# Kernel tuning notes

Hardware: AMD Instinct MI355X
Metric: run time of the kernel (lower is better)

## Reference

```python
import jax, jax.numpy as jnp
import numpy as np

CHANNELS = 25
BN_EPS = 1e-5


def _diff(x):
    # x: [B,H,W]; zero-pad by 1 on H and W, then shifted slices (same as torch diff())
    xp = jnp.pad(x, ((0, 0), (1, 1), (1, 1)))
    p_x = (xp[:, 2:, 1:-1] - xp[:, :-2, 1:-1]) / 2
    p_y = (xp[:, 1:-1, 2:] - xp[:, 1:-1, :-2]) / 2
    pp_x = xp[:, 2:, 1:-1] + xp[:, :-2, 1:-1] - 2 * x
    pp_y = xp[:, 1:-1, 2:] + xp[:, 1:-1, :-2] - 2 * x
    pp_xy = xp[:, 2:, 2:] + xp[:, :-2, :-2] - xp[:, 2:, 1:-1] - xp[:, 1:-1, 2:]
    return p_x, p_y, pp_x, pp_y, pp_xy


def _batchnorm(x, gamma, beta):
    # x: [B,C,H,W]; training-mode BN with batch statistics (biased variance)
    mean = jnp.mean(x, axis=(0, 2, 3), keepdims=True)
    var = jnp.mean((x - mean) ** 2, axis=(0, 2, 3), keepdims=True)
    xhat = (x - mean) * jax.lax.rsqrt(var + BN_EPS)
    return xhat * gamma[None, :, None, None] + beta[None, :, None, None]


def setup_inputs() -> dict:
    key = jax.random.key(0)
    ks = jax.random.split(key, 5)
    B, H, W = 32, 512, 512
    x = jax.random.normal(ks[0], (B, H, W), dtype=jnp.float32)
    # 1x1 conv weights stored as [out_ch, in_ch]
    w1 = jax.random.normal(ks[1], (CHANNELS, 6), dtype=jnp.float32) * (1.0 / np.sqrt(6.0))
    b1 = jnp.zeros((CHANNELS,), dtype=jnp.float32)
    g1 = jnp.ones((CHANNELS,), dtype=jnp.float32)
    beta1 = jnp.zeros((CHANNELS,), dtype=jnp.float32)
    w2 = jax.random.normal(ks[2], (1, CHANNELS), dtype=jnp.float32) * (1.0 / np.sqrt(CHANNELS))
    b2 = jnp.zeros((1,), dtype=jnp.float32)
    g2 = jnp.ones((1,), dtype=jnp.float32)
    beta2 = jnp.zeros((1,), dtype=jnp.float32)
    return {"x": x, "w1": w1, "b1": b1, "g1": g1, "beta1": beta1,
            "w2": w2, "b2": b2, "g2": g2, "beta2": beta2}


def reference(x, w1, b1, g1, beta1, w2, b2, g2, beta2):
    p_x, p_y, pp_x, pp_y, pp_xy = _diff(x)
    xx = jnp.stack([x, p_x, p_y, pp_x, pp_y, pp_xy], axis=1)  # [B,6,H,W]
    # 1x1 conv == per-pixel channel matmul
    h = jnp.einsum('bchw,oc->bohw', xx, w1) + b1[None, :, None, None]
    h = jax.nn.relu(_batchnorm(h, g1, beta1))  # [B,25,H,W]
    o = jnp.einsum('bchw,oc->bohw', h, w2) + b2[None, :, None, None]
    o = jax.nn.relu(_batchnorm(o, g2, beta2))[:, 0, :, :]  # [B,H,W]
    return o + x
```

## Files before the change

kernel.cpp:

```cpp
#include <hip/hip_runtime.h>
#include <hip/hip_fp16.h>

typedef float f4 __attribute__((ext_vector_type(4)));
typedef float f2 __attribute__((ext_vector_type(2)));
typedef _Float16 f16x8 __attribute__((ext_vector_type(8)));
typedef float f32x16 __attribute__((ext_vector_type(16)));

#define NPIX (32*512*512)
#define BN_EPS 1e-5f


__global__ __launch_bounds__(256) void k_moments(const float* __restrict__ x,
                                                 const float* __restrict__ ws,
                                                 float* __restrict__ outp) {
    __shared__ ushort sl[4][8][64];
    __shared__ float mom[4][7][7];
    int t = threadIdx.x;
    int l = t & 63, wv = t >> 6;
    int h = l >> 5;
    const float* zb = ws + 1024;

    sl[wv][6][l] = (ushort)0x3C00;
    sl[wv][7][l] = (ushort)0;

    f32x16 accA, accB;
    #pragma unroll
    for (int r = 0; r < 16; ++r) { accA[r] = 0.f; accB[r] = 0.f; }

    int arow = ((l & 31) < 7) ? (l & 31) : 7;
    const ushort* rdp = &sl[wv][arow][8*h];

    int wave_id = blockIdx.x * 4 + wv;
    #pragma unroll 1
    for (int rr = 0; rr < 2; ++rr) {
        int row = wave_id * 2 + rr;
        int i = row & 511;
        const float* xr = x + row * 512;
        const float* xn = (i > 0)   ? xr - 512 : zb;
        const float* xs = (i < 511) ? xr + 512 : zb;
        #pragma unroll 1
        for (int it = 0; it < 8; ++it) {
            int col = it * 64 + l;
            bool okw = (col > 0), oke = (col < 511);
            int cm = okw ? col - 1 : 0;
            int cp = oke ? col + 1 : 511;
            float C  = xr[col], N = xn[col], S_ = xs[col];
            float W_ = xr[cm],  E = xr[cp];
            float NW = xn[cm],  SE = xs[cp];
            W_ = okw ? W_ : 0.f; NW = okw ? NW : 0.f;
            E  = oke ? E  : 0.f; SE = oke ? SE : 0.f;

            float s0 = C;
            float s1 = (S_ - N) * 0.5f;
            float s2 = (E - W_) * 0.5f;
            float s3 = S_ + N - 2.f*C;
            float s4 = E + W_ - 2.f*C;
            float s5 = SE + NW - S_ - E;

            __half h0 = __float2half(s0), h1 = __float2half(s1);
            __half h2 = __float2half(s2), h3 = __float2half(s3);
            __half h4 = __float2half(s4), h5 = __float2half(s5);
            sl[wv][0][l] = *(ushort*)&h0;
            sl[wv][1][l] = *(ushort*)&h1;
            sl[wv][2][l] = *(ushort*)&h2;
            sl[wv][3][l] = *(ushort*)&h3;
            sl[wv][4][l] = *(ushort*)&h4;
            sl[wv][5][l] = *(ushort*)&h5;
            __builtin_amdgcn_wave_barrier();

            union { uint4 u; f16x8 v; } f0, f1, f2_, f3;
            f0.u  = *(const uint4*)(rdp);
            f1.u  = *(const uint4*)(rdp + 16);
            f2_.u = *(const uint4*)(rdp + 32);
            f3.u  = *(const uint4*)(rdp + 48);
            accA = __builtin_amdgcn_mfma_f32_32x32x16_f16(f0.v,  f0.v,  accA, 0, 0, 0);
            accB = __builtin_amdgcn_mfma_f32_32x32x16_f16(f1.v,  f1.v,  accB, 0, 0, 0);
            accA = __builtin_amdgcn_mfma_f32_32x32x16_f16(f2_.v, f2_.v, accA, 0, 0, 0);
            accB = __builtin_amdgcn_mfma_f32_32x32x16_f16(f3.v,  f3.v,  accB, 0, 0, 0);
            __builtin_amdgcn_wave_barrier();
        }
    }

    if ((l & 31) < 7) {
        int j = l & 31;
        #pragma unroll
        for (int r = 0; r < 4; ++r) {
            int irow = r + 4*h;
            if (irow < 7) mom[wv][irow][j] = accA[r] + accB[r];
        }
    }
    __syncthreads();
    if (t < 27) {
        int a, b;
        if (t < 6) { a = t; b = 6; }
        else {
            int rem = t - 6; a = 0;
            while (rem >= 6 - a) { rem -= 6 - a; ++a; }
            b = a + rem;
        }
        float v = mom[0][a][b] + mom[1][a][b] + mom[2][a][b] + mom[3][a][b];
        outp[t*2048 + blockIdx.x] = v;
    }
}

__global__ __launch_bounds__(256) void k_red(const float* __restrict__ outp,
                                             float* __restrict__ ws) {
    int b = blockIdx.x;
    int t = threadIdx.x;
    float v = 0.f;
    #pragma unroll
    for (int k = 0; k < 8; ++k) v += outp[b*2048 + t + 256*k];
    for (int off = 32; off; off >>= 1) v += __shfl_xor(v, off);
    __shared__ float red[4];
    int wave = t >> 6, lane = t & 63;
    if (lane == 0) red[wave] = v;
    __syncthreads();
    if (t == 0) ws[b] = red[0] + red[1] + red[2] + red[3];
}

__global__ void k_stats1(const float* w1, const float* b1, const float* g1,
                         const float* beta1, const float* w2, float* ws) {
    __shared__ float sm[32][8];
    int c = threadIdx.x;
    if (c < 32) {
        #pragma unroll
        for (int k = 0; k < 8; ++k) sm[c][k] = 0.f;
        ws[64 + c] = (c < 25) ? w2[c] : 0.f;
    }
    __syncthreads();
    if (c < 25) {
        const float invN = 1.f / (float)NPIX;
        float m1[6], wr[6];
        #pragma unroll
        for (int i = 0; i < 6; ++i) m1[i] = ws[i] * invN;
        #pragma unroll
        for (int i = 0; i < 6; ++i) wr[i] = w1[c*6 + i];
        float bc = b1[c];
        float mean = bc;
        #pragma unroll
        for (int i = 0; i < 6; ++i) mean = fmaf(wr[i], m1[i], mean);
        float e2 = bc * bc;
        #pragma unroll
        for (int i = 0; i < 6; ++i) e2 = fmaf(2.f*bc*wr[i], m1[i], e2);
        #pragma unroll
        for (int i = 0; i < 6; ++i)
            #pragma unroll
            for (int j = 0; j < 6; ++j) {
                int a = i < j ? i : j, b = i < j ? j : i;
                float m2 = ws[6 + a*(11-a)/2 + b] * invN;
                e2 = fmaf(wr[i]*wr[j], m2, e2);
            }
        float var = e2 - mean*mean;
        float a1 = g1[c] * rsqrtf(var + BN_EPS);
        #pragma unroll
        for (int i = 0; i < 6; ++i) sm[c][i] = a1 * wr[i];
        sm[c][6] = fmaf(a1, bc - mean, beta1[c]);
    }
    __syncthreads();
    int ch = c & 31, h = c >> 5;
    float aC=0.f, aN=0.f, aS=0.f, aE=0.f, aW=0.f, aNW=0.f, aSE=0.f, ab=0.f;
    if (h == 0) {
        float w0 = sm[ch][0], w1v = sm[ch][1], w2v = sm[ch][2];
        float w3 = sm[ch][3], w4v = sm[ch][4], w5 = sm[ch][5], be = sm[ch][6];
        aC  = w0 - 2.f*w3 - 2.f*w4v;
        aN  = -0.5f*w1v + w3;
        aS  =  0.5f*w1v + w3 - w5;
        aE  =  0.5f*w2v + w4v - w5;
        aW  = -0.5f*w2v + w4v;
        aNW = w5;
        aSE = w5;
        ab  = be;
    }
    __half2 p0 = __floats2half2_rn(aC,  aN);
    __half2 p1 = __floats2half2_rn(aS,  aE);
    __half2 p2 = __floats2half2_rn(aW,  aNW);
    __half2 p3 = __floats2half2_rn(aSE, ab);
    unsigned u0, u1, u2, u3;
    __builtin_memcpy(&u0, &p0, 4);
    __builtin_memcpy(&u1, &p1, 4);
    __builtin_memcpy(&u2, &p2, 4);
    __builtin_memcpy(&u3, &p3, 4);
    uint4 fr = {u0, u1, u2, u3};
    ((uint4*)(ws + 96))[c] = fr;
}

__global__ __launch_bounds__(256) void k_main(const float* __restrict__ x,
                                              const float* __restrict__ ws,
                                              const float* __restrict__ b2,
                                              float* __restrict__ stats,
                                              float* __restrict__ opre) {
    int t = threadIdx.x;
    int l = t & 63, wv = t >> 6;
    int lane31 = l & 31, h = l >> 5;
    const float* zb = ws + 1024;

    f16x8 afr;
    {
        uint4 u = ((const uint4*)(ws + 96))[l];
        union { uint4 u; f16x8 v; } cv; cv.u = u; afr = cv.v;
    }
    f2 w2p[8];
    #pragma unroll
    for (int r2 = 0; r2 < 8; ++r2) {
        int creg = ((2*r2) & 3) + 8 * ((2*r2) >> 2) + 4*h;
        w2p[r2] = *(const f2*)(ws + 64 + creg);
    }
    f32x16 zacc;
    #pragma unroll
    for (int r = 0; r < 16; ++r) zacc[r] = 0.f;
    float b2v = b2[0];
    float S1 = 0.f, S2 = 0.f;

    int wave_id = blockIdx.x * 4 + wv;
    #pragma unroll 1
    for (int rr = 0; rr < 2; ++rr) {
        int row = wave_id * 2 + rr;
        int i = row & 511;
        const float* xc = x + row * 512 + lane31;
        const float* xn = (i > 0)   ? xc - 512 : zb + lane31;
        const float* xs = (i < 511) ? xc + 512 : zb + lane31;
        float* op = opre + row * 512 + lane31;

        #pragma unroll
        for (int jt = 0; jt < 16; ++jt) {
            const int o4 = jt * 32;
            int offm1 = o4 - 1, offp1 = o4 + 1;
            if (jt == 0  && lane31 == 0)  offm1 = o4;
            if (jt == 15 && lane31 == 31) offp1 = o4;

            float C  = xc[o4];
            float W_ = xc[offm1];
            float E  = xc[offp1];
            float N  = xn[o4];
            float NW = xn[offm1];
            float S_ = xs[o4];
            float SE = xs[offp1];
            if (jt == 0)  { bool ok = (lane31 != 0);  W_ = ok ? W_ : 0.f; NW = ok ? NW : 0.f; }
            if (jt == 15) { bool ok = (lane31 != 31); E  = ok ? E  : 0.f; SE = ok ? SE : 0.f; }

            __half2 p0 = __floats2half2_rn(C,  N);
            __half2 p1 = __floats2half2_rn(S_, E);
            __half2 p2 = __floats2half2_rn(W_, NW);
            __half2 p3 = __floats2half2_rn(SE, 1.f);
            unsigned u0, u1, u2, u3;
            __builtin_memcpy(&u0, &p0, 4);
            __builtin_memcpy(&u1, &p1, 4);
            __builtin_memcpy(&u2, &p2, 4);
            __builtin_memcpy(&u3, &p3, 4);
            union { uint4 u; f16x8 v; } bv;
            bv.u = (uint4){u0, u1, u2, u3};

            f32x16 acc = __builtin_amdgcn_mfma_f32_32x32x16_f16(afr, bv.v, zacc, 0, 0, 0);

            f2 oa = {0.f, 0.f};
            #pragma unroll
            for (int r2 = 0; r2 < 8; ++r2) {
                f2 rel;
                rel.x = fmaxf(acc[2*r2],   0.f);
                rel.y = fmaxf(acc[2*r2+1], 0.f);
                asm("v_pk_fma_f32 %0, %1, %2, %0" : "+v"(oa) : "v"(rel), "v"(w2p[r2]));
            }
            float o = oa.x + oa.y;
            o += __shfl_xor(o, 32);
            o += b2v;
            S1 += o;
            S2 = fmaf(o, o, S2);
            if (l < 32) op[o4] = o;
        }
    }

    for (int off = 32; off; off >>= 1) { S1 += __shfl_xor(S1, off); S2 += __shfl_xor(S2, off); }
    __shared__ float red[2][4];
    if (l == 0) { red[0][wv] = S1; red[1][wv] = S2; }
    __syncthreads();
    if (t == 0) stats[2048 + blockIdx.x] = 0.5f*(red[0][0]+red[0][1]+red[0][2]+red[0][3]);
    if (t == 1) stats[4096 + blockIdx.x] = 0.5f*(red[1][0]+red[1][1]+red[1][2]+red[1][3]);
}

__global__ __launch_bounds__(256) void k_redS(float* __restrict__ ws) {
    int t = threadIdx.x;
    float s1 = 0.f, s2 = 0.f;
    #pragma unroll
    for (int k = 0; k < 8; ++k) {
        s1 += ws[2048 + t + 256*k];
        s2 += ws[4096 + t + 256*k];
    }
    for (int off = 32; off; off >>= 1) { s1 += __shfl_xor(s1, off); s2 += __shfl_xor(s2, off); }
    __shared__ float red[2][4];
    int wave = t >> 6, lane = t & 63;
    if (lane == 0) { red[0][wave] = s1; red[1][wave] = s2; }
    __syncthreads();
    if (t == 0) ws[27] = red[0][0] + red[0][1] + red[0][2] + red[0][3];
    if (t == 1) ws[28] = red[1][0] + red[1][1] + red[1][2] + red[1][3];
}

__global__ __launch_bounds__(256) void k_final(const float* __restrict__ x,
                                               const float* __restrict__ ws,
                                               const float* __restrict__ g2,
                                               const float* __restrict__ beta2,
                                               float* __restrict__ out) {
    const float invN = 1.f / (float)NPIX;
    float mean = ws[27] * invN;
    float var  = ws[28] * invN - mean*mean;
    float a2 = g2[0] * rsqrtf(var + BN_EPS);
    float c2 = fmaf(-mean, a2, beta2[0]);

    int idx = blockIdx.x * 256 + threadIdx.x;
    f4 o  = ((const f4*)out)[idx];
    f4 xv = ((const f4*)x)[idx];
    f4 r;
    r.x = fmaxf(fmaf(a2, o.x, c2), 0.f) + xv.x;
    r.y = fmaxf(fmaf(a2, o.y, c2), 0.f) + xv.y;
    r.z = fmaxf(fmaf(a2, o.z, c2), 0.f) + xv.z;
    r.w = fmaxf(fmaf(a2, o.w, c2), 0.f) + xv.w;
    ((f4*)out)[idx] = r;
}

extern "C" void kernel_launch(void* const* d_in, const int* in_sizes, int n_in,
                              void* d_out, int out_size, void* d_ws, size_t ws_size,
                              hipStream_t stream) {
    const float* x     = (const float*)d_in[0];
    const float* w1    = (const float*)d_in[1];
    const float* b1    = (const float*)d_in[2];
    const float* g1    = (const float*)d_in[3];
    const float* beta1 = (const float*)d_in[4];
    const float* w2    = (const float*)d_in[5];
    const float* b2    = (const float*)d_in[6];
    const float* g2    = (const float*)d_in[7];
    const float* beta2 = (const float*)d_in[8];
    float* out = (float*)d_out;
    float* ws  = (float*)d_ws;

    hipMemsetAsync(ws, 0, 8192, stream);
    k_moments<<<2048, 256, 0, stream>>>(x, ws, out);
    k_red    <<<27, 256, 0, stream>>>(out, ws);
    k_stats1 <<<1, 64, 0, stream>>>(w1, b1, g1, beta1, w2, ws);
    k_main   <<<2048, 256, 0, stream>>>(x, ws, b2, ws, out);
    k_redS   <<<1, 256, 0, stream>>>(ws);
    k_final  <<<8192, 256, 0, stream>>>(x, ws, g2, beta2, out);
}
```

Measured before the change: 102.1 us.

## Fuse moment reduction into stats kernel, batch two column tiles per LDS sync, scalarize output FMA

The separate 27-block reduction kernel is merged into the single-block stats kernel, which now loops over all 27 moment sums itself, removing one launch. The moments kernel processes 128 columns per iteration, with a doubled LDS buffer, so the wave barriers and loop overhead are paid half as often. In the main kernel, the packed v_pk_fma inline asm is replaced by a plain scalar fmaf chain over 16 accumulators. The fused reduction runs serially in one block with 54 __syncthreads, which may cost more than the removed launch. The scalar FMA chain has a longer dependency chain than the packed version.

Measured after the change: 112.4 us. 10.2% more time.

```diff
diff --git a/kernel.cpp b/kernel.cpp
--- a/kernel.cpp
+++ b/kernel.cpp
@@ -13,22 +13,24 @@
 __global__ __launch_bounds__(256) void k_moments(const float* __restrict__ x,
                                                  const float* __restrict__ ws,
                                                  float* __restrict__ outp) {
-    __shared__ ushort sl[4][8][64];
+    __shared__ ushort sl[4][8][128];
     __shared__ float mom[4][7][7];
     int t = threadIdx.x;
     int l = t & 63, wv = t >> 6;
     int h = l >> 5;
     const float* zb = ws + 1024;
 
-    sl[wv][6][l] = (ushort)0x3C00;
-    sl[wv][7][l] = (ushort)0;
+    sl[wv][6][l]      = (ushort)0x3C00;
+    sl[wv][6][l + 64] = (ushort)0x3C00;
+    sl[wv][7][l]      = (ushort)0;
+    sl[wv][7][l + 64] = (ushort)0;
 
     f32x16 accA, accB;
     #pragma unroll
     for (int r = 0; r < 16; ++r) { accA[r] = 0.f; accB[r] = 0.f; }
 
     int arow = ((l & 31) < 7) ? (l & 31) : 7;
-    const ushort* rdp = &sl[wv][arow][8*h];
+    const ushort* rbase = &sl[wv][arow][8*h];
 
     int wave_id = blockIdx.x * 4 + wv;
     #pragma unroll 1
@@ -39,44 +41,52 @@
         const float* xn = (i > 0)   ? xr - 512 : zb;
         const float* xs = (i < 511) ? xr + 512 : zb;
         #pragma unroll 1
-        for (int it = 0; it < 8; ++it) {
-            int col = it * 64 + l;
-            bool okw = (col > 0), oke = (col < 511);
-            int cm = okw ? col - 1 : 0;
-            int cp = oke ? col + 1 : 511;
-            float C  = xr[col], N = xn[col], S_ = xs[col];
-            float W_ = xr[cm],  E = xr[cp];
-            float NW = xn[cm],  SE = xs[cp];
-            W_ = okw ? W_ : 0.f; NW = okw ? NW : 0.f;
-            E  = oke ? E  : 0.f; SE = oke ? SE : 0.f;
-
-            float s0 = C;
-            float s1 = (S_ - N) * 0.5f;
-            float s2 = (E - W_) * 0.5f;
-            float s3 = S_ + N - 2.f*C;
-            float s4 = E + W_ - 2.f*C;
-            float s5 = SE + NW - S_ - E;
-
-            __half h0 = __float2half(s0), h1 = __float2half(s1);
-            __half h2 = __float2half(s2), h3 = __float2half(s3);
-            __half h4 = __float2half(s4), h5 = __float2half(s5);
-            sl[wv][0][l] = *(ushort*)&h0;
-            sl[wv][1][l] = *(ushort*)&h1;
-            sl[wv][2][l] = *(ushort*)&h2;
-            sl[wv][3][l] = *(ushort*)&h3;
-            sl[wv][4][l] = *(ushort*)&h4;
-            sl[wv][5][l] = *(ushort*)&h5;
+        for (int it = 0; it < 4; ++it) {
+            #pragma unroll
+            for (int half = 0; half < 2; ++half) {
+                int col = it * 128 + half * 64 + l;
+                bool okw = (col > 0), oke = (col < 511);
+                int cm = okw ? col - 1 : 0;
+                int cp = oke ? col + 1 : 511;
+                float C  = xr[col], N = xn[col], S_ = xs[col];
+                float W_ = xr[cm],  E = xr[cp];
+                float NW = xn[cm],  SE = xs[cp];
+                W_ = okw ? W_ : 0.f; NW = okw ? NW : 0.f;
+                E  = oke ? E  : 0.f; SE = oke ? SE : 0.f;
+
+                float s0 = C;
+                float s1 = (S_ - N) * 0.5f;
+                float s2 = (E - W_) * 0.5f;
+                float s3 = S_ + N - 2.f*C;
+                float s4 = E + W_ - 2.f*C;
+                float s5 = SE + NW - S_ - E;
+
+                int px = half * 64 + l;
+                __half h0 = __float2half(s0), h1 = __float2half(s1);
+                __half h2 = __float2half(s2), h3 = __float2half(s3);
+                __half h4 = __float2half(s4), h5 = __float2half(s5);
+                sl[wv][0][px] = *(ushort*)&h0;
+                sl[wv][1][px] = *(ushort*)&h1;
+                sl[wv][2][px] = *(ushort*)&h2;
+                sl[wv][3][px] = *(ushort*)&h3;
+                sl[wv][4][px] = *(ushort*)&h4;
+                sl[wv][5][px] = *(ushort*)&h5;
+            }
             __builtin_amdgcn_wave_barrier();
 
-            union { uint4 u; f16x8 v; } f0, f1, f2_, f3;
-            f0.u  = *(const uint4*)(rdp);
-            f1.u  = *(const uint4*)(rdp + 16);
-            f2_.u = *(const uint4*)(rdp + 32);
-            f3.u  = *(const uint4*)(rdp + 48);
-            accA = __builtin_amdgcn_mfma_f32_32x32x16_f16(f0.v,  f0.v,  accA, 0, 0, 0);
-            accB = __builtin_amdgcn_mfma_f32_32x32x16_f16(f1.v,  f1.v,  accB, 0, 0, 0);
-            accA = __builtin_amdgcn_mfma_f32_32x32x16_f16(f2_.v, f2_.v, accA, 0, 0, 0);
-            accB = __builtin_amdgcn_mfma_f32_32x32x16_f16(f3.v,  f3.v,  accB, 0, 0, 0);
+            #pragma unroll
+            for (int m = 0; m < 2; ++m) {
+                union { uint4 u; f16x8 v; } f0, f1, f2_, f3;
+                const ushort* rdp = rbase + 64*m;
+                f0.u  = *(const uint4*)(rdp);
+                f1.u  = *(const uint4*)(rdp + 16);
+                f2_.u = *(const uint4*)(rdp + 32);
+                f3.u  = *(const uint4*)(rdp + 48);
+                accA = __builtin_amdgcn_mfma_f32_32x32x16_f16(f0.v,  f0.v,  accA, 0, 0, 0);
+                accB = __builtin_amdgcn_mfma_f32_32x32x16_f16(f1.v,  f1.v,  accB, 0, 0, 0);
+                accA = __builtin_amdgcn_mfma_f32_32x32x16_f16(f2_.v, f2_.v, accA, 0, 0, 0);
+                accB = __builtin_amdgcn_mfma_f32_32x32x16_f16(f3.v,  f3.v,  accB, 0, 0, 0);
+            }
             __builtin_amdgcn_wave_barrier();
         }
     }
@@ -103,25 +113,29 @@
     }
 }
 
-__global__ __launch_bounds__(256) void k_red(const float* __restrict__ outp,
-                                             float* __restrict__ ws) {
-    int b = blockIdx.x;
+__global__ __launch_bounds__(256) void k_stats1(const float* __restrict__ outp,
+                                                const float* w1, const float* b1,
+                                                const float* g1, const float* beta1,
+                                                const float* w2, float* ws) {
+    __shared__ float sm[32][8];
+    __shared__ float redsm[27];
     int t = threadIdx.x;
-    float v = 0.f;
-    #pragma unroll
-    for (int k = 0; k < 8; ++k) v += outp[b*2048 + t + 256*k];
-    for (int off = 32; off; off >>= 1) v += __shfl_xor(v, off);
-    __shared__ float red[4];
-    int wave = t >> 6, lane = t & 63;
-    if (lane == 0) red[wave] = v;
-    __syncthreads();
-    if (t == 0) ws[b] = red[0] + red[1] + red[2] + red[3];
-}
-
-__global__ void k_stats1(const float* w1, const float* b1, const float* g1,
-                         const float* beta1, const float* w2, float* ws) {
-    __shared__ float sm[32][8];
-    int c = threadIdx.x;
+
+    #pragma unroll 1
+    for (int b = 0; b < 27; ++b) {
+        float v = 0.f;
+        #pragma unroll
+        for (int k = 0; k < 8; ++k) v += outp[b*2048 + t + 256*k];
+        for (int off = 32; off; off >>= 1) v += __shfl_xor(v, off);
+        __shared__ float red4[4];
+        if ((t & 63) == 0) red4[t >> 6] = v;
+        __syncthreads();
+        if (t == 0) redsm[b] = red4[0] + red4[1] + red4[2] + red4[3];
+        __syncthreads();
+    }
+    if (t < 27) ws[t] = redsm[t];
+
+    int c = t;
     if (c < 32) {
         #pragma unroll
         for (int k = 0; k < 8; ++k) sm[c][k] = 0.f;
@@ -132,7 +146,7 @@
         const float invN = 1.f / (float)NPIX;
         float m1[6], wr[6];
         #pragma unroll
-        for (int i = 0; i < 6; ++i) m1[i] = ws[i] * invN;
+        for (int i = 0; i < 6; ++i) m1[i] = redsm[i] * invN;
         #pragma unroll
         for (int i = 0; i < 6; ++i) wr[i] = w1[c*6 + i];
         float bc = b1[c];
@@ -147,7 +161,7 @@
             #pragma unroll
             for (int j = 0; j < 6; ++j) {
                 int a = i < j ? i : j, b = i < j ? j : i;
-                float m2 = ws[6 + a*(11-a)/2 + b] * invN;
+                float m2 = redsm[6 + a*(11-a)/2 + b] * invN;
                 e2 = fmaf(wr[i]*wr[j], m2, e2);
             }
         float var = e2 - mean*mean;
@@ -157,31 +171,33 @@
         sm[c][6] = fmaf(a1, bc - mean, beta1[c]);
     }
     __syncthreads();
-    int ch = c & 31, h = c >> 5;
-    float aC=0.f, aN=0.f, aS=0.f, aE=0.f, aW=0.f, aNW=0.f, aSE=0.f, ab=0.f;
-    if (h == 0) {
-        float w0 = sm[ch][0], w1v = sm[ch][1], w2v = sm[ch][2];
-        float w3 = sm[ch][3], w4v = sm[ch][4], w5 = sm[ch][5], be = sm[ch][6];
-        aC  = w0 - 2.f*w3 - 2.f*w4v;
-        aN  = -0.5f*w1v + w3;
-        aS  =  0.5f*w1v + w3 - w5;
-        aE  =  0.5f*w2v + w4v - w5;
-        aW  = -0.5f*w2v + w4v;
-        aNW = w5;
-        aSE = w5;
-        ab  = be;
-    }
-    __half2 p0 = __floats2half2_rn(aC,  aN);
-    __half2 p1 = __floats2half2_rn(aS,  aE);
-    __half2 p2 = __floats2half2_rn(aW,  aNW);
-    __half2 p3 = __floats2half2_rn(aSE, ab);
-    unsigned u0, u1, u2, u3;
-    __builtin_memcpy(&u0, &p0, 4);
-    __builtin_memcpy(&u1, &p1, 4);
-    __builtin_memcpy(&u2, &p2, 4);
-    __builtin_memcpy(&u3, &p3, 4);
-    uint4 fr = {u0, u1, u2, u3};
-    ((uint4*)(ws + 96))[c] = fr;
+    if (c < 64) {
+        int ch = c & 31, h = c >> 5;
+        float aC=0.f, aN=0.f, aS=0.f, aE=0.f, aW=0.f, aNW=0.f, aSE=0.f, ab=0.f;
+        if (h == 0) {
+            float w0 = sm[ch][0], w1v = sm[ch][1], w2v = sm[ch][2];
+            float w3 = sm[ch][3], w4v = sm[ch][4], w5 = sm[ch][5], be = sm[ch][6];
+            aC  = w0 - 2.f*w3 - 2.f*w4v;
+            aN  = -0.5f*w1v + w3;
+            aS  =  0.5f*w1v + w3 - w5;
+            aE  =  0.5f*w2v + w4v - w5;
+            aW  = -0.5f*w2v + w4v;
+            aNW = w5;
+            aSE = w5;
+            ab  = be;
+        }
+        __half2 p0 = __floats2half2_rn(aC,  aN);
+        __half2 p1 = __floats2half2_rn(aS,  aE);
+        __half2 p2 = __floats2half2_rn(aW,  aNW);
+        __half2 p3 = __floats2half2_rn(aSE, ab);
+        unsigned u0, u1, u2, u3;
+        __builtin_memcpy(&u0, &p0, 4);
+        __builtin_memcpy(&u1, &p1, 4);
+        __builtin_memcpy(&u2, &p2, 4);
+        __builtin_memcpy(&u3, &p3, 4);
+        uint4 fr = {u0, u1, u2, u3};
+        ((uint4*)(ws + 96))[c] = fr;
+    }
 }
 
 __global__ __launch_bounds__(256) void k_main(const float* __restrict__ x,
@@ -199,11 +215,11 @@
         uint4 u = ((const uint4*)(ws + 96))[l];
         union { uint4 u; f16x8 v; } cv; cv.u = u; afr = cv.v;
     }
-    f2 w2p[8];
+    float w2v[16];
     #pragma unroll
-    for (int r2 = 0; r2 < 8; ++r2) {
-        int creg = ((2*r2) & 3) + 8 * ((2*r2) >> 2) + 4*h;
-        w2p[r2] = *(const f2*)(ws + 64 + creg);
+    for (int r = 0; r < 16; ++r) {
+        int creg = (r & 3) + 8 * (r >> 2);
+        w2v[r] = ws[64 + creg + 4*h];
     }
     f32x16 zacc;
     #pragma unroll
@@ -252,15 +268,10 @@
 
             f32x16 acc = __builtin_amdgcn_mfma_f32_32x32x16_f16(afr, bv.v, zacc, 0, 0, 0);
 
-            f2 oa = {0.f, 0.f};
+            float o = 0.f;
             #pragma unroll
-            for (int r2 = 0; r2 < 8; ++r2) {
-                f2 rel;
-                rel.x = fmaxf(acc[2*r2],   0.f);
-                rel.y = fmaxf(acc[2*r2+1], 0.f);
-                asm("v_pk_fma_f32 %0, %1, %2, %0" : "+v"(oa) : "v"(rel), "v"(w2p[r2]));
-            }
-            float o = oa.x + oa.y;
+            for (int r = 0; r < 16; ++r)
+                o = fmaf(fmaxf(acc[r], 0.f), w2v[r], o);
             o += __shfl_xor(o, 32);
             o += b2v;
             S1 += o;
@@ -333,8 +344,7 @@
 
     hipMemsetAsync(ws, 0, 8192, stream);
     k_moments<<<2048, 256, 0, stream>>>(x, ws, out);
-    k_red    <<<27, 256, 0, stream>>>(out, ws);
-    k_stats1 <<<1, 64, 0, stream>>>(w1, b1, g1, beta1, w2, ws);
+    k_stats1 <<<1, 256, 0, stream>>>(out, w1, b1, g1, beta1, w2, ws);
     k_main   <<<2048, 256, 0, stream>>>(x, ws, b2, ws, out);
     k_redS   <<<1, 256, 0, stream>>>(ws);
     k_final  <<<8192, 256, 0, stream>>>(x, ws, g2, beta2, out);
```
